# Kernel tuning notes

Measured on AMD Instinct MI355X. Metric: run time of the kernel, lower is better.

## Reference

```python
import jax, jax.numpy as jnp
import numpy as np

D_MODEL = 1024
NHEAD = 16
D_FF = 4096
LN_EPS = 1e-5


def _layer_norm(x, g, b):
    mu = jnp.mean(x, axis=-1, keepdims=True)
    var = jnp.mean(jnp.square(x - mu), axis=-1, keepdims=True)
    return (x - mu) * jax.lax.rsqrt(var + LN_EPS) * g + b


def setup_inputs() -> dict:
    key = jax.random.key(0)
    ks = jax.random.split(key, 12)
    d, f = D_MODEL, D_FF
    s = 1.0 / np.sqrt(d)
    inp = {
        "src": jax.random.normal(ks[0], (2, 2048, d), dtype=jnp.float32),
        "Wq": jax.random.uniform(ks[1], (d, d), jnp.float32, -s, s),
        "bq": jnp.zeros((d,), jnp.float32),
        "Wk": jax.random.uniform(ks[2], (d, d), jnp.float32, -s, s),
        "bk": jnp.zeros((d,), jnp.float32),
        "Wv": jax.random.uniform(ks[3], (d, d), jnp.float32, -s, s),
        "bv": jnp.zeros((d,), jnp.float32),
        "Wo": jax.random.uniform(ks[4], (d, d), jnp.float32, -s, s),
        "bo": jnp.zeros((d,), jnp.float32),
        "W1": jax.random.uniform(ks[5], (d, f), jnp.float32, -s, s),
        "b1": jnp.zeros((f,), jnp.float32),
        "W2": jax.random.uniform(ks[6], (f, d), jnp.float32, -1.0 / np.sqrt(f), 1.0 / np.sqrt(f)),
        "b2": jnp.zeros((d,), jnp.float32),
        "ln1_g": jnp.ones((d,), jnp.float32),
        "ln1_b": jnp.zeros((d,), jnp.float32),
        "ln2_g": jnp.ones((d,), jnp.float32),
        "ln2_b": jnp.zeros((d,), jnp.float32),
    }
    return inp


def reference(src, Wq, bq, Wk, bk, Wv, bv, Wo, bo, W1, b1, W2, b2,
              ln1_g, ln1_b, ln2_g, ln2_b):
    B, S, D = src.shape
    H = NHEAD
    hd = D // H
    # QKV projections, split into heads: [B, H, S, hd]
    q = (src @ Wq + bq).reshape(B, S, H, hd).transpose(0, 2, 1, 3)
    k = (src @ Wk + bk).reshape(B, S, H, hd).transpose(0, 2, 1, 3)
    v = (src @ Wv + bv).reshape(B, S, H, hd).transpose(0, 2, 1, 3)
    # Explicit full-score attention (no mask branch), as in source.
    scores = jnp.einsum("bhqd,bhkd->bhqk", q, k) / jnp.sqrt(jnp.asarray(hd, src.dtype))
    attn = jax.nn.softmax(scores, axis=-1)
    ctx = jnp.einsum("bhqk,bhkd->bhqd", attn, v)
    ctx = ctx.transpose(0, 2, 1, 3).reshape(B, S, D)
    src2 = ctx @ Wo + bo
    x = _layer_norm(src + src2, ln1_g, ln1_b)
    ff = jax.nn.relu(x @ W1 + b1) @ W2 + b2
    out = _layer_norm(x + ff, ln2_g, ln2_b)
    return out
```

## Files before the change

### kernel.cpp

```cpp
#include <hip/hip_runtime.h>
#include <cstdint>
#include <cstddef>

#define SEQ 2048
#define BATCH 2
#define ROWS (BATCH * SEQ)

typedef __attribute__((ext_vector_type(8))) short short8;
typedef __attribute__((ext_vector_type(4))) float f32x4;
typedef __attribute__((ext_vector_type(8))) _Float16 half8;
typedef __attribute__((ext_vector_type(2))) __fp16 fp16x2;

__device__ __forceinline__ unsigned short f2bf(float f) {
  union { float f; uint32_t u; } v; v.f = f;
  uint32_t r = v.u + 0x7fffu + ((v.u >> 16) & 1u);
  return (unsigned short)(r >> 16);
}

__device__ __forceinline__ unsigned short bf2h(unsigned short b) {
  union { uint32_t u; float f; } v; v.u = ((uint32_t)b) << 16;
  union { _Float16 h; unsigned short u; } o; o.h = (_Float16)v.f;
  return o.u;
}

__device__ __forceinline__ void async16(const void* g, void* l) {
  __builtin_amdgcn_global_load_lds((const __attribute__((address_space(1))) void*)g,
                                   (__attribute__((address_space(3))) void*)l, 16, 0, 0);
}

__global__ __launch_bounds__(256) void f2bf_kernel(const float* __restrict__ in,
                                                   unsigned short* __restrict__ out) {
  size_t i = ((size_t)blockIdx.x * 256 + threadIdx.x) * 4;
  float4 vv = *(const float4*)(in + i);
  ushort4 o;
  o.x = f2bf(vv.x); o.y = f2bf(vv.y); o.z = f2bf(vv.z); o.w = f2bf(vv.w);
  *(ushort4*)(out + i) = o;
}

__global__ __launch_bounds__(256) void wtrans(const float* __restrict__ W,
                                              unsigned short* __restrict__ WT,
                                              int K, int N, float scale) {
  __shared__ float t[32][33];
  int n0 = blockIdx.x * 32, k0 = blockIdx.y * 32;
  for (int i = threadIdx.y; i < 32; i += 8)
    t[i][threadIdx.x] = W[(size_t)(k0 + i) * N + n0 + threadIdx.x];
  __syncthreads();
  for (int i = threadIdx.y; i < 32; i += 8)
    WT[(size_t)(n0 + i) * K + k0 + threadIdx.x] = f2bf(t[threadIdx.x][i] * scale);
}

__global__ __launch_bounds__(256) void bias_concat(const float* __restrict__ bq,
                                                   const float* __restrict__ bk,
                                                   const float* __restrict__ bv,
                                                   float* __restrict__ o) {
  int i = blockIdx.x * 256 + threadIdx.x;
  float v = (i < 1024) ? bq[i] * 0.18033688f : (i < 2048 ? bk[i - 1024] : bv[i - 2048]);
  o[i] = v;
}

__global__ __launch_bounds__(256) void vtrans(const unsigned short* __restrict__ qkv,
                                              unsigned short* __restrict__ VT) {
  const int st = blockIdx.x, bh = blockIdx.y, b = bh >> 4, h = bh & 15;
  __shared__ unsigned short t[64][72];
  const int tid = threadIdx.x;
#pragma unroll
  for (int it = 0; it < 2; ++it) {
    int i = it * 256 + tid;
    int s = i >> 3, c = (i & 7) * 8;
    short8 v = *(const short8*)(qkv + ((size_t)b * SEQ + st * 64 + s) * 3072 + 2048 + h * 64 + c);
#pragma unroll
    for (int j = 0; j < 8; ++j) t[c + j][s] = bf2h((unsigned short)v[j]);
  }
  __syncthreads();
#pragma unroll
  for (int it = 0; it < 2; ++it) {
    int i = it * 256 + tid;
    int d = i >> 3, sc = (i & 7) * 8;
    short8 o;
#pragma unroll
    for (int j = 0; j < 8; ++j) o[j] = (short)t[d][sc + j];
    *(short8*)(VT + ((size_t)bh * 64 + d) * 2048 + st * 64 + sc) = o;
  }
}

template <bool RELU, bool OUTBF, bool HASRES>
__global__ __launch_bounds__(256) void gemm_bt(
    const unsigned short* __restrict__ A, const unsigned short* __restrict__ BT,
    const float* __restrict__ bias, const float* __restrict__ Rres,
    float* __restrict__ outF, unsigned short* __restrict__ outB,
    int M, int N, int K) {
  __shared__ unsigned short As[2][128 * 32];
  __shared__ unsigned short Bs[2][128 * 32];
  const int tid = threadIdx.x;
  const int lane = tid & 63, ln = lane & 15, quad = lane >> 4;
  const int w = tid >> 6;
  const int m0 = blockIdx.y * 128, n0 = blockIdx.x * 128;
  const int mw = (w >> 1) * 64, nw = (w & 1) * 64;
  f32x4 acc[4][4] = {};
  const int i0 = tid, i1 = tid + 256;
  const int r0 = i0 >> 2, kc0 = (i0 & 3) * 8;
  const int r1 = i1 >> 2, kc1 = (i1 & 3) * 8;
  for (int k0 = 0; k0 < K; k0 += 64) {
    __syncthreads();
#pragma unroll
    for (int p = 0; p < 2; ++p) {
      const int kp = k0 + p * 32;
      async16(A + (size_t)(m0 + r0) * K + kp + kc0, &As[p][i0 * 8]);
      async16(A + (size_t)(m0 + r1) * K + kp + kc1, &As[p][i1 * 8]);
      async16(BT + (size_t)(n0 + r0) * K + kp + kc0, &Bs[p][i0 * 8]);
      async16(BT + (size_t)(n0 + r1) * K + kp + kc1, &Bs[p][i1 * 8]);
    }
    __syncthreads();
#pragma unroll
    for (int p = 0; p < 2; ++p) {
      short8 a[4], b[4];
#pragma unroll
      for (int mi = 0; mi < 4; ++mi)
        a[mi] = *(const short8*)&As[p][(mw + mi * 16 + ln) * 32 + quad * 8];
#pragma unroll
      for (int ni = 0; ni < 4; ++ni)
        b[ni] = *(const short8*)&Bs[p][(nw + ni * 16 + ln) * 32 + quad * 8];
#pragma unroll
      for (int mi = 0; mi < 4; ++mi)
#pragma unroll
        for (int ni = 0; ni < 4; ++ni)
          acc[mi][ni] = __builtin_amdgcn_mfma_f32_16x16x32_bf16(a[mi], b[ni], acc[mi][ni], 0, 0, 0);
    }
  }
#pragma unroll
  for (int mi = 0; mi < 4; ++mi) {
#pragma unroll
    for (int ni = 0; ni < 4; ++ni) {
#pragma unroll
      for (int reg = 0; reg < 4; ++reg) {
        int row = m0 + mw + mi * 16 + quad * 4 + reg;
        int col = n0 + nw + ni * 16 + ln;
        float v = acc[mi][ni][reg] + bias[col];
        if (HASRES) v += Rres[(size_t)row * N + col];
        if (RELU) v = fmaxf(v, 0.f);
        if (OUTBF) outB[(size_t)row * N + col] = f2bf(v);
        else outF[(size_t)row * N + col] = v;
      }
    }
  }
}

template <bool RELU, bool OUTBF, bool HASRES>
__global__ __launch_bounds__(256) void gemm_bt64(
    const unsigned short* __restrict__ A, const unsigned short* __restrict__ BT,
    const float* __restrict__ bias, const float* __restrict__ Rres,
    float* __restrict__ outF, unsigned short* __restrict__ outB,
    int M, int N, int K) {
  __shared__ unsigned short As[4][128 * 32];
  __shared__ unsigned short Bs[4][64 * 32];
  const int tid = threadIdx.x;
  const int lane = tid & 63, ln = lane & 15, quad = lane >> 4;
  const int w = tid >> 6;
  const int m0 = blockIdx.y * 128, n0 = blockIdx.x * 64;
  const int mw = w * 32;
  f32x4 acc[2][4] = {};
  const int i0 = tid, i1 = tid + 256;
  const int r0 = i0 >> 2, kc0 = (i0 & 3) * 8;
  const int r1 = i1 >> 2, kc1 = (i1 & 3) * 8;
  for (int k0 = 0; k0 < K; k0 += 128) {
    __syncthreads();
#pragma unroll
    for (int p = 0; p < 4; ++p) {
      const int kp = k0 + p * 32;
      async16(A + (size_t)(m0 + r0) * K + kp + kc0, &As[p][i0 * 8]);
      async16(A + (size_t)(m0 + r1) * K + kp + kc1, &As[p][i1 * 8]);
      async16(BT + (size_t)(n0 + r0) * K + kp + kc0, &Bs[p][i0 * 8]);
    }
    __syncthreads();
#pragma unroll
    for (int p = 0; p < 4; ++p) {
      short8 a[2], b[4];
#pragma unroll
      for (int mi = 0; mi < 2; ++mi)
        a[mi] = *(const short8*)&As[p][(mw + mi * 16 + ln) * 32 + quad * 8];
#pragma unroll
      for (int ni = 0; ni < 4; ++ni)
        b[ni] = *(const short8*)&Bs[p][(ni * 16 + ln) * 32 + quad * 8];
#pragma unroll
      for (int mi = 0; mi < 2; ++mi)
#pragma unroll
        for (int ni = 0; ni < 4; ++ni)
          acc[mi][ni] = __builtin_amdgcn_mfma_f32_16x16x32_bf16(a[mi], b[ni], acc[mi][ni], 0, 0, 0);
    }
  }
#pragma unroll
  for (int mi = 0; mi < 2; ++mi) {
#pragma unroll
    for (int ni = 0; ni < 4; ++ni) {
#pragma unroll
      for (int reg = 0; reg < 4; ++reg) {
        int row = m0 + mw + mi * 16 + quad * 4 + reg;
        int col = n0 + ni * 16 + ln;
        float v = acc[mi][ni][reg] + bias[col];
        if (HASRES) v += Rres[(size_t)row * N + col];
        if (RELU) v = fmaxf(v, 0.f);
        if (OUTBF) outB[(size_t)row * N + col] = f2bf(v);
        else outF[(size_t)row * N + col] = v;
      }
    }
  }
}

__global__ __launch_bounds__(256, 4) void attn_kernel(const unsigned short* __restrict__ qkv,
                                                      const unsigned short* __restrict__ VT,
                                                      unsigned short* __restrict__ ctx) {
  const int qt = blockIdx.x;
  const int bh = blockIdx.y, b = bh >> 4, h = bh & 15;
  const int tid = threadIdx.x;
  const int w = tid >> 6, lane = tid & 63, ln = lane & 15, quad = lane >> 4;
  __shared__ __align__(16) unsigned short Qs[4096];
  __shared__ __align__(16) unsigned short Ks[4096];
  __shared__ __align__(16) unsigned short Vs[4096];
  __shared__ __align__(16) unsigned short Ps[4096];
  const size_t rowbase = (size_t)b * SEQ;
  const unsigned short* kbase = qkv + (rowbase)*3072 + 1024 + h * 64;
  const unsigned short* vbase = VT + (size_t)bh * 64 * 2048;
  const int r0 = tid >> 3, c0 = tid & 7;
  const int r1 = r0 + 32;
  const int sw0 = r0 * 64 + ((c0 ^ (r0 & 7)) * 8);
  const int sw1 = r1 * 64 + ((c0 ^ (r1 & 7)) * 8);
  {
    const unsigned short* qb = qkv + (rowbase + qt * 64) * 3072 + h * 64;
#pragma unroll
    for (int it = 0; it < 2; ++it) {
      int i = it * 256 + tid;
      int r = i >> 3, c = (i & 7) * 8;
      *(short8*)&Qs[r * 64 + (((i & 7) ^ (r & 7)) * 8)] =
          *(const short8*)(qb + (size_t)r * 3072 + c);
    }
  }
  short8 kreg0 = *(const short8*)(kbase + (size_t)r0 * 3072 + c0 * 8);
  short8 kreg1 = *(const short8*)(kbase + (size_t)r1 * 3072 + c0 * 8);
  short8 vreg0 = *(const short8*)(vbase + (size_t)r0 * 2048 + c0 * 8);
  short8 vreg1 = *(const short8*)(vbase + (size_t)r1 * 2048 + c0 * 8);
  *(short8*)&Ks[sw0] = kreg0;
  *(short8*)&Ks[sw1] = kreg1;
  *(short8*)&Vs[sw0] = vreg0;
  *(short8*)&Vs[sw1] = vreg1;
  __syncthreads();
  const int lh = ln & 7;
  const int qrow = w * 16 + ln;
  short8 aq0 = *(const short8*)&Qs[qrow * 64 + ((0 + quad) ^ lh) * 8];
  short8 aq1 = *(const short8*)&Qs[qrow * 64 + ((4 + quad) ^ lh) * 8];
  f32x4 oacc[4] = {};
  float lsum[4] = {};
  const int pr0 = ln * 64 + ((0 + quad) ^ lh) * 8;
  const int pr1 = ln * 64 + ((4 + quad) ^ lh) * 8;
  unsigned short* Pw = &Ps[w * 1024];
  for (int kt = 0; kt < 32; ++kt) {
    if (kt < 31) {
      const unsigned short* kp = kbase + (size_t)(kt + 1) * 64 * 3072;
      const unsigned short* vp = vbase + (kt + 1) * 64;
      kreg0 = *(const short8*)(kp + (size_t)r0 * 3072 + c0 * 8);
      kreg1 = *(const short8*)(kp + (size_t)r1 * 3072 + c0 * 8);
      vreg0 = *(const short8*)(vp + (size_t)r0 * 2048 + c0 * 8);
      vreg1 = *(const short8*)(vp + (size_t)r1 * 2048 + c0 * 8);
    }
#pragma unroll
    for (int nt = 0; nt < 4; ++nt) {
      short8 bk0 = *(const short8*)&Ks[(nt * 16 + ln) * 64 + ((0 + quad) ^ lh) * 8];
      short8 bk1 = *(const short8*)&Ks[(nt * 16 + ln) * 64 + ((4 + quad) ^ lh) * 8];
      const int pc = nt * 2 + (ln >> 3);
      const int q4 = quad * 4;
      f32x4 z = {};
      z = __builtin_amdgcn_mfma_f32_16x16x32_bf16(aq0, bk0, z, 0, 0, 0);
      z = __builtin_amdgcn_mfma_f32_16x16x32_bf16(aq1, bk1, z, 0, 0, 0);
      float p0 = __builtin_amdgcn_exp2f(z[0]);
      float p1 = __builtin_amdgcn_exp2f(z[1]);
      float p2 = __builtin_amdgcn_exp2f(z[2]);
      float p3 = __builtin_amdgcn_exp2f(z[3]);
      lsum[0] += p0; lsum[1] += p1; lsum[2] += p2; lsum[3] += p3;
      union { fp16x2 h; unsigned short u[2]; } ca, cb;
      ca.h = __builtin_amdgcn_cvt_pkrtz(p0, p1);
      cb.h = __builtin_amdgcn_cvt_pkrtz(p2, p3);
      Pw[(q4 + 0) * 64 + ((pc ^ ((q4 + 0) & 7)) * 8) + lh] = ca.u[0];
      Pw[(q4 + 1) * 64 + ((pc ^ ((q4 + 1) & 7)) * 8) + lh] = ca.u[1];
      Pw[(q4 + 2) * 64 + ((pc ^ ((q4 + 2) & 7)) * 8) + lh] = cb.u[0];
      Pw[(q4 + 3) * 64 + ((pc ^ ((q4 + 3) & 7)) * 8) + lh] = cb.u[1];
    }
    asm volatile("s_waitcnt lgkmcnt(0)" ::: "memory");
    half8 ap0 = *(const half8*)&Pw[pr0];
    half8 ap1 = *(const half8*)&Pw[pr1];
#pragma unroll
    for (int ot = 0; ot < 4; ++ot) {
      half8 bv0 = *(const half8*)&Vs[(ot * 16 + ln) * 64 + ((0 + quad) ^ lh) * 8];
      half8 bv1 = *(const half8*)&Vs[(ot * 16 + ln) * 64 + ((4 + quad) ^ lh) * 8];
      oacc[ot] = __builtin_amdgcn_mfma_f32_16x16x32_f16(ap0, bv0, oacc[ot], 0, 0, 0);
      oacc[ot] = __builtin_amdgcn_mfma_f32_16x16x32_f16(ap1, bv1, oacc[ot], 0, 0, 0);
    }
    if (kt < 31) {
      __syncthreads();
      *(short8*)&Ks[sw0] = kreg0;
      *(short8*)&Ks[sw1] = kreg1;
      *(short8*)&Vs[sw0] = vreg0;
      *(short8*)&Vs[sw1] = vreg1;
      __syncthreads();
    }
  }
  {
    float rl[4];
#pragma unroll
    for (int r = 0; r < 4; ++r) {
      float l = lsum[r];
#pragma unroll
      for (int off = 1; off < 16; off <<= 1) l += __shfl_xor(l, off);
      rl[r] = 1.0f / l;
    }
#pragma unroll
    for (int ot = 0; ot < 4; ++ot)
#pragma unroll
      for (int r = 0; r < 4; ++r) {
        int srow = qt * 64 + w * 16 + quad * 4 + r;
        int c = h * 64 + ot * 16 + ln;
        ctx[(rowbase + srow) * 1024 + c] = f2bf(oacc[ot][r] * rl[r]);
      }
  }
}

__global__ __launch_bounds__(256) void ln_kernel(const float* __restrict__ y,
                                                 const float* __restrict__ g,
                                                 const float* __restrict__ bb,
                                                 float* __restrict__ outF,
                                                 unsigned short* __restrict__ outB) {
  const int row = blockIdx.x;
  const int tid = threadIdx.x;
  const float* yr = y + (size_t)row * 1024;
  float v[4]; float s = 0.f, s2 = 0.f;
#pragma unroll
  for (int j = 0; j < 4; ++j) {
    v[j] = yr[tid + j * 256];
    s += v[j]; s2 += v[j] * v[j];
  }
#pragma unroll
  for (int off = 1; off < 64; off <<= 1) {
    s += __shfl_xor(s, off);
    s2 += __shfl_xor(s2, off);
  }
  __shared__ float ws1[4], ws2[4];
  if ((tid & 63) == 0) { ws1[tid >> 6] = s; ws2[tid >> 6] = s2; }
  __syncthreads();
  s = ws1[0] + ws1[1] + ws1[2] + ws1[3];
  s2 = ws2[0] + ws2[1] + ws2[2] + ws2[3];
  const float mu = s * (1.f / 1024.f);
  const float var = s2 * (1.f / 1024.f) - mu * mu;
  const float rstd = rsqrtf(var + 1e-5f);
#pragma unroll
  for (int j = 0; j < 4; ++j) {
    int c = tid + j * 256;
    float val = (v[j] - mu) * rstd * g[c] + bb[c];
    if (outF) outF[(size_t)row * 1024 + c] = val;
    if (outB) outB[(size_t)row * 1024 + c] = f2bf(val);
  }
}

extern "C" void kernel_launch(void* const* d_in, const int* in_sizes, int n_in,
                              void* d_out, int out_size, void* d_ws, size_t ws_size,
                              hipStream_t stream) {
  const float* src = (const float*)d_in[0];
  const float* Wq = (const float*)d_in[1];
  const float* bq = (const float*)d_in[2];
  const float* Wk = (const float*)d_in[3];
  const float* bk = (const float*)d_in[4];
  const float* Wv = (const float*)d_in[5];
  const float* bv = (const float*)d_in[6];
  const float* Wo = (const float*)d_in[7];
  const float* bo = (const float*)d_in[8];
  const float* W1 = (const float*)d_in[9];
  const float* b1 = (const float*)d_in[10];
  const float* W2 = (const float*)d_in[11];
  const float* b2 = (const float*)d_in[12];
  const float* ln1g = (const float*)d_in[13];
  const float* ln1b = (const float*)d_in[14];
  const float* ln2g = (const float*)d_in[15];
  const float* ln2b = (const float*)d_in[16];
  float* out = (float*)d_out;

  char* ws = (char*)d_ws;
  unsigned short* qkvT = (unsigned short*)(ws + 0);
  unsigned short* WoT  = (unsigned short*)(ws + 6291456);
  unsigned short* W1T  = (unsigned short*)(ws + 8388608);
  unsigned short* W2T  = (unsigned short*)(ws + 16777216);
  float*          biasq = (float*)(ws + 25165824);
  unsigned short* xbf  = (unsigned short*)(ws + 25178112);
  unsigned short* qkv  = (unsigned short*)(ws + 33566720);
  unsigned short* hbuf = qkv;
  unsigned short* ctx  = (unsigned short*)(ws + 58732544);
  float*          ybuf = (float*)(ws + 67121152);
  unsigned short* VT   = (unsigned short*)(ws + 67121152);
  float*          xf   = (float*)(ws + 83898368);

  const float QSCALE = 0.18033688f;

  f2bf_kernel<<<4096, 256, 0, stream>>>(src, xbf);
  wtrans<<<dim3(32, 32), dim3(32, 8), 0, stream>>>(Wq, qkvT, 1024, 1024, QSCALE);
  wtrans<<<dim3(32, 32), dim3(32, 8), 0, stream>>>(Wk, qkvT + 1024 * 1024, 1024, 1024, 1.0f);
  wtrans<<<dim3(32, 32), dim3(32, 8), 0, stream>>>(Wv, qkvT + 2048 * 1024, 1024, 1024, 1.0f);
  wtrans<<<dim3(32, 32), dim3(32, 8), 0, stream>>>(Wo, WoT, 1024, 1024, 1.0f);
  wtrans<<<dim3(128, 32), dim3(32, 8), 0, stream>>>(W1, W1T, 1024, 4096, 1.0f);
  wtrans<<<dim3(32, 128), dim3(32, 8), 0, stream>>>(W2, W2T, 4096, 1024, 1.0f);
  bias_concat<<<12, 256, 0, stream>>>(bq, bk, bv, biasq);

  gemm_bt<false, true, false><<<dim3(24, 32), 256, 0, stream>>>(
      xbf, qkvT, biasq, nullptr, nullptr, qkv, ROWS, 3072, 1024);
  vtrans<<<dim3(32, 32), 256, 0, stream>>>(qkv, VT);
  attn_kernel<<<dim3(32, 32), 256, 0, stream>>>(qkv, VT, ctx);
  gemm_bt64<false, false, true><<<dim3(16, 32), 256, 0, stream>>>(
      ctx, WoT, bo, src, ybuf, nullptr, ROWS, 1024, 1024);
  ln_kernel<<<4096, 256, 0, stream>>>(ybuf, ln1g, ln1b, xf, xbf);
  gemm_bt<true, true, false><<<dim3(32, 32), 256, 0, stream>>>(
      xbf, W1T, b1, nullptr, nullptr, hbuf, ROWS, 4096, 1024);
  gemm_bt64<false, false, true><<<dim3(16, 32), 256, 0, stream>>>(
      hbuf, W2T, b2, xf, ybuf, nullptr, ROWS, 1024, 4096);
  ln_kernel<<<4096, 256, 0, stream>>>(ybuf, ln2g, ln2b, out, nullptr);
}
```

Baseline: 400.4 us.

## Double-buffer K/V tiles in attention, load Q directly to registers, add MFMA priority

The attention kernel now keeps two LDS buffers for K and V, so the next tile is written into the alternate buffer and one of the two __syncthreads per iteration goes away. Q fragments are read straight from global memory into registers, which removes the Qs shared buffer and its staging. s_setprio is raised around MFMA groups so matrix instructions get issue priority. LDS use rises from 32KB to 40KB per block, which may lower occupancy, and the Q loads are no longer coalesced.

```diff
diff --git a/kernel.cpp b/kernel.cpp
--- a/kernel.cpp
+++ b/kernel.cpp
@@ -213,9 +213,8 @@
   const int bh = blockIdx.y, b = bh >> 4, h = bh & 15;
   const int tid = threadIdx.x;
   const int w = tid >> 6, lane = tid & 63, ln = lane & 15, quad = lane >> 4;
-  __shared__ __align__(16) unsigned short Qs[4096];
-  __shared__ __align__(16) unsigned short Ks[4096];
-  __shared__ __align__(16) unsigned short Vs[4096];
+  __shared__ __align__(16) unsigned short Ks[2 * 4096];
+  __shared__ __align__(16) unsigned short Vs[2 * 4096];
   __shared__ __align__(16) unsigned short Ps[4096];
   const size_t rowbase = (size_t)b * SEQ;
   const unsigned short* kbase = qkv + (rowbase)*3072 + 1024 + h * 64;
@@ -224,16 +223,11 @@
   const int r1 = r0 + 32;
   const int sw0 = r0 * 64 + ((c0 ^ (r0 & 7)) * 8);
   const int sw1 = r1 * 64 + ((c0 ^ (r1 & 7)) * 8);
-  {
-    const unsigned short* qb = qkv + (rowbase + qt * 64) * 3072 + h * 64;
-#pragma unroll
-    for (int it = 0; it < 2; ++it) {
-      int i = it * 256 + tid;
-      int r = i >> 3, c = (i & 7) * 8;
-      *(short8*)&Qs[r * 64 + (((i & 7) ^ (r & 7)) * 8)] =
-          *(const short8*)(qb + (size_t)r * 3072 + c);
-    }
-  }
+  const int lh = ln & 7;
+  const int qrow = w * 16 + ln;
+  const unsigned short* qb = qkv + (rowbase + qt * 64) * 3072 + h * 64;
+  short8 aq0 = *(const short8*)(qb + (size_t)qrow * 3072 + quad * 8);
+  short8 aq1 = *(const short8*)(qb + (size_t)qrow * 3072 + 32 + quad * 8);
   short8 kreg0 = *(const short8*)(kbase + (size_t)r0 * 3072 + c0 * 8);
   short8 kreg1 = *(const short8*)(kbase + (size_t)r1 * 3072 + c0 * 8);
   short8 vreg0 = *(const short8*)(vbase + (size_t)r0 * 2048 + c0 * 8);
@@ -243,15 +237,12 @@
   *(short8*)&Vs[sw0] = vreg0;
   *(short8*)&Vs[sw1] = vreg1;
   __syncthreads();
-  const int lh = ln & 7;
-  const int qrow = w * 16 + ln;
-  short8 aq0 = *(const short8*)&Qs[qrow * 64 + ((0 + quad) ^ lh) * 8];
-  short8 aq1 = *(const short8*)&Qs[qrow * 64 + ((4 + quad) ^ lh) * 8];
   f32x4 oacc[4] = {};
   float lsum[4] = {};
   const int pr0 = ln * 64 + ((0 + quad) ^ lh) * 8;
   const int pr1 = ln * 64 + ((4 + quad) ^ lh) * 8;
   unsigned short* Pw = &Ps[w * 1024];
+  int bsel = 0;
   for (int kt = 0; kt < 32; ++kt) {
     if (kt < 31) {
       const unsigned short* kp = kbase + (size_t)(kt + 1) * 64 * 3072;
@@ -261,15 +252,19 @@
       vreg0 = *(const short8*)(vp + (size_t)r0 * 2048 + c0 * 8);
       vreg1 = *(const short8*)(vp + (size_t)r1 * 2048 + c0 * 8);
     }
+    const unsigned short* Kb = &Ks[bsel];
+    const unsigned short* Vb = &Vs[bsel];
 #pragma unroll
     for (int nt = 0; nt < 4; ++nt) {
-      short8 bk0 = *(const short8*)&Ks[(nt * 16 + ln) * 64 + ((0 + quad) ^ lh) * 8];
-      short8 bk1 = *(const short8*)&Ks[(nt * 16 + ln) * 64 + ((4 + quad) ^ lh) * 8];
+      short8 bk0 = *(const short8*)&Kb[(nt * 16 + ln) * 64 + ((0 + quad) ^ lh) * 8];
+      short8 bk1 = *(const short8*)&Kb[(nt * 16 + ln) * 64 + ((4 + quad) ^ lh) * 8];
       const int pc = nt * 2 + (ln >> 3);
       const int q4 = quad * 4;
       f32x4 z = {};
+      __builtin_amdgcn_s_setprio(1);
       z = __builtin_amdgcn_mfma_f32_16x16x32_bf16(aq0, bk0, z, 0, 0, 0);
       z = __builtin_amdgcn_mfma_f32_16x16x32_bf16(aq1, bk1, z, 0, 0, 0);
+      __builtin_amdgcn_s_setprio(0);
       float p0 = __builtin_amdgcn_exp2f(z[0]);
       float p1 = __builtin_amdgcn_exp2f(z[1]);
       float p2 = __builtin_amdgcn_exp2f(z[2]);
@@ -288,17 +283,19 @@
     half8 ap1 = *(const half8*)&Pw[pr1];
 #pragma unroll
     for (int ot = 0; ot < 4; ++ot) {
-      half8 bv0 = *(const half8*)&Vs[(ot * 16 + ln) * 64 + ((0 + quad) ^ lh) * 8];
-      half8 bv1 = *(const half8*)&Vs[(ot * 16 + ln) * 64 + ((4 + quad) ^ lh) * 8];
+      half8 bv0 = *(const half8*)&Vb[(ot * 16 + ln) * 64 + ((0 + quad) ^ lh) * 8];
+      half8 bv1 = *(const half8*)&Vb[(ot * 16 + ln) * 64 + ((4 + quad) ^ lh) * 8];
+      __builtin_amdgcn_s_setprio(1);
       oacc[ot] = __builtin_amdgcn_mfma_f32_16x16x32_f16(ap0, bv0, oacc[ot], 0, 0, 0);
       oacc[ot] = __builtin_amdgcn_mfma_f32_16x16x32_f16(ap1, bv1, oacc[ot], 0, 0, 0);
+      __builtin_amdgcn_s_setprio(0);
     }
     if (kt < 31) {
-      __syncthreads();
-      *(short8*)&Ks[sw0] = kreg0;
-      *(short8*)&Ks[sw1] = kreg1;
-      *(short8*)&Vs[sw0] = vreg0;
-      *(short8*)&Vs[sw1] = vreg1;
+      bsel ^= 4096;
+      *(short8*)&Ks[bsel + sw0] = kreg0;
+      *(short8*)&Ks[bsel + sw1] = kreg1;
+      *(short8*)&Vs[bsel + sw0] = vreg0;
+      *(short8*)&Vs[bsel + sw1] = vreg1;
       __syncthreads();
     }
   }
```

Measured after the change: 394.1 us. About the same (-1.6%).
